# Optimization experiments

Hardware: AMD Instinct MI355X
Metric: run time of the kernel (lower is better)

The kernel has to match this reference:

```python
import jax, jax.numpy as jnp
import numpy as np

B, T, C, H, W = 16, 8, 2048, 16, 8
C8, C4, HW, NP = C // 8, C // 4, H * W, T // 2


def _cbr(x, w, s, b):
    # 1x1 conv + folded BN (eval-mode affine) + ReLU; x: (N, Cin, H, W), w: (Cout, Cin)
    y = jnp.einsum('oc,nchw->nohw', w, x)
    return jax.nn.relu(y * s[None, :, None, None] + b[None, :, None, None])


def setup_inputs():
    key = jax.random.key(0)
    ks = jax.random.split(key, 16)
    r = lambda i, shape, sc: jax.random.normal(ks[i], shape, jnp.float32) * sc
    return dict(
        featmap=r(0, (B, T, C, H, W), 1.0),
        re_featmap=r(1, (B * T, C, H, W), 1.0),
        vect_featmap=r(2, (B, T, C), 1.0),
        embed_feat=r(3, (B, T, 128, H, W), 1.0),
        gamma_w=r(4, (C8, C), 0.03), gamma_s=jnp.ones((C8,)), gamma_b=jnp.zeros((C8,)),
        beta_w=r(5, (C8, C), 0.03), beta_s=jnp.ones((C8,)), beta_b=jnp.zeros((C8,)),
        gg_w=r(6, (128, 2 * HW), 0.05), gg_s=jnp.ones((128,)), gg_b=jnp.zeros((128,)),
        tte_w=r(7, (128, 256), 0.05), tte_s=jnp.ones((128,)), tte_b=jnp.zeros((128,)),
        te_w=r(8, (1, 256), 0.05), te_s=jnp.ones((1,)), te_b=jnp.zeros((1,)),
        theta_w=r(9, (C8, C), 0.03), theta_b=jnp.zeros((C8,)),
        cp_w1=r(10, (C8, C4), 0.05), cp_b1=jnp.zeros((C8,)),
        cp_w2=r(11, (C, C8), 0.05), cp_b2=jnp.zeros((C,)),
    )


def reference(featmap, re_featmap, vect_featmap, embed_feat,
              gamma_w, gamma_s, gamma_b, beta_w, beta_s, beta_b,
              gg_w, gg_s, gg_b, tte_w, tte_s, tte_b, te_w, te_s, te_b,
              theta_w, theta_b, cp_w1, cp_b1, cp_w2, cp_b2):
    # spatial attention embeddings: (B, T, C8, HW)
    gamma = _cbr(re_featmap, gamma_w, gamma_s, gamma_b).reshape(B, T, C8, HW)
    beta = _cbr(re_featmap, beta_w, beta_s, beta_b).reshape(B, T, C8, HW)

    # channel attention: Conv1d over time of (B, C, T) -> (B, C8, T)
    cp = jax.nn.relu(jnp.einsum('oc,btc->bot', theta_w, vect_featmap) + theta_b[None, :, None])
    cp = cp.reshape(B, C8, NP, 2)
    c0 = cp[..., 0].transpose(0, 2, 1)  # (B, NP, C8)
    c1 = cp[..., 1].transpose(0, 2, 1)

    def mlp(x):  # (B, NP, C4) -> sigmoid gate (B, NP, C)
        h1 = jax.nn.relu(x @ cp_w1.T + cp_b1)
        return jax.nn.sigmoid(h1 @ cp_w2.T + cp_b2)

    p00 = mlp(jnp.concatenate([c0, c1], -1))  # (B, NP, C)
    p01 = mlp(jnp.concatenate([c1, c0], -1))

    # pairwise spatial graphs
    g0, g1 = gamma[:, 0::2], gamma[:, 1::2]  # (B, NP, C8, HW)
    b0, b1 = beta[:, 0::2], beta[:, 1::2]
    Gs0 = jnp.einsum('bpcs,bpct->bpst', g0, b1)  # (B, NP, HW, HW)
    Gs1 = jnp.einsum('bpcs,bpct->bpst', g1, b0)
    # Gs_in = Gs^T viewed as (HW, H, W); Gs_out = Gs viewed likewise
    j0 = jnp.concatenate([Gs0.transpose(0, 1, 3, 2), Gs1], 2).reshape(B * NP, 2 * HW, H, W)
    j1 = jnp.concatenate([Gs1.transpose(0, 1, 3, 2), Gs0], 2).reshape(B * NP, 2 * HW, H, W)
    gj0 = _cbr(j0, gg_w, gg_s, gg_b)  # (B*NP, 128, H, W)
    gj1 = _cbr(j1, gg_w, gg_s, gg_b)

    ef = embed_feat.reshape(B, NP, 2, 128, H, W)
    e0 = ef[:, :, 0].reshape(B * NP, 128, H, W)
    e1 = ef[:, :, 1].reshape(B * NP, 128, H, W)
    ta = _cbr(jnp.concatenate([e0, e1], 1), tte_w, tte_s, tte_b)  # (B*NP, 128, H, W)
    tb = _cbr(jnp.concatenate([e1, e0], 1), tte_w, tte_s, tte_b)

    def gate(t_feat, gj):  # conv 256->1 + BN + sigmoid
        y = jnp.einsum('oc,nchw->nohw', te_w, jnp.concatenate([t_feat, gj], 1))
        return jax.nn.sigmoid(y * te_s[None, :, None, None] + te_b[None, :, None, None])

    pa = gate(ta, gj0).reshape(B, NP, 1, H, W)
    pb = gate(tb, gj1).reshape(B, NP, 1, H, W)

    f = featmap.reshape(B, NP, 2, C, H, W)
    gate0 = p00[..., None, None] * pa  # (B, NP, C, H, W)
    gate1 = p01[..., None, None] * pb
    out = jax.nn.relu(gate0 * f[:, :, 0] + gate1 * f[:, :, 1])
    return out * out  # (B, T//2, C, H, W)
```

## Files before the change

### kernel.cpp

```cpp
#include <hip/hip_runtime.h>
#include <stdint.h>


typedef _Float16 f16;
typedef _Float16 f16x8 __attribute__((ext_vector_type(8)));
typedef float f32x4 __attribute__((ext_vector_type(4)));

typedef const void __attribute__((address_space(1)))* gptr1;
typedef void __attribute__((address_space(3)))* lptr3;

__device__ __forceinline__ void gload16(const void* g, void* l) {
  __builtin_amdgcn_global_load_lds((gptr1)g, (lptr3)l, 16, 0, 0);
}

__device__ __forceinline__ float sigmoidf_(float x) { return 1.f / (1.f + expf(-x)); }

#define WAIT_VM6 asm volatile("s_waitcnt vmcnt(6)" ::: "memory")
#define WAIT_VM0 asm volatile("s_waitcnt vmcnt(0)" ::: "memory")
#define WAIT_LGKM8 asm volatile("s_waitcnt lgkmcnt(8)" ::: "memory")
#define WAIT_LGKM0 asm volatile("s_waitcnt lgkmcnt(0)" ::: "memory")

__global__ __launch_bounds__(256) void kPP(const float* __restrict__ x,
                                           f16* __restrict__ Af,
                                           const float* __restrict__ gw, const float* __restrict__ gs,
                                           const float* __restrict__ bw, const float* __restrict__ bs,
                                           const float* __restrict__ gg_w, const float* __restrict__ gg_s,
                                           const float* __restrict__ tte_w, const float* __restrict__ tte_s,
                                           const float* __restrict__ thw, const float* __restrict__ w1,
                                           const float* __restrict__ w2,
                                           f16* __restrict__ Wf,
                                           float* __restrict__ ggT, float* __restrict__ tteT,
                                           float* __restrict__ thwT, float* __restrict__ w1T,
                                           float* __restrict__ w2T) {
  __shared__ __align__(16) char shmem[64 * 129 * 4];
  int t = threadIdx.x;
  int bid = blockIdx.x;
  if (bid < 4096) {
    float (*L)[129] = (float(*)[129])shmem;
    int n = bid >> 5;
    int k0 = (bid & 31) * 64;
    const float* src = x + (size_t)n * 262144 + (size_t)k0 * 128;
    for (int r = 0; r < 8; ++r) {
      int f = r * 256 + t;
      int kk = f >> 5, c4 = (f & 31) * 4;
      float4 v = *(const float4*)(src + kk * 128 + c4);
      L[kk][c4 + 0] = v.x; L[kk][c4 + 1] = v.y; L[kk][c4 + 2] = v.z; L[kk][c4 + 3] = v.w;
    }
    __syncthreads();
    for (int r = 0; r < 4; ++r) {
      int id = r * 256 + t;
      int hw = id >> 3, c = id & 7;
      int cs = c ^ (hw & 7);
      f16x8 h8;
      for (int j = 0; j < 8; ++j)
        h8[j] = (f16)L[cs * 8 + j][hw];
      size_t m = (size_t)n * 128 + hw;
      size_t ob = m * 2048 + (size_t)k0 + (size_t)c * 8;
      *(f16x8*)(Af + ob) = h8;
    }
    return;
  }
  if (bid < 4608) {
    int id = (bid - 4096) * 256 + t;
    int o = id >> 8, cch = id & 255;
    float s; const float* row;
    if (o < 256) { s = gs[o]; row = gw + (size_t)o * 2048; }
    else         { s = bs[o - 256]; row = bw + (size_t)(o - 256) * 2048; }
    int kb = cch >> 3, sub = cch & 7;
    int subd = sub ^ (o & 7);
    f16x8 h8;
    for (int j = 0; j < 8; ++j)
      h8[j] = (f16)(row[cch * 8 + j] * s);
    size_t ob = (size_t)o * 2048 + (size_t)kb * 64 + (size_t)subd * 8;
    *(f16x8*)(Wf + ob) = h8;
    return;
  }
  float (*TL)[65] = (float(*)[65])shmem;
  int tb = bid - 4608;
  const float* src; float* dst; const float* scale = nullptr; int R, C;
  if (tb < 128)      { src = thw;   dst = thwT; R = 256;  C = 2048; }
  else if (tb < 256) { tb -= 128; src = w2;  dst = w2T;  R = 2048; C = 256; }
  else if (tb < 288) { tb -= 256; src = w1;  dst = w1T;  R = 256;  C = 512; }
  else if (tb < 296) { tb -= 288; src = gg_w;  dst = ggT;  scale = gg_s;  R = 128; C = 256; }
  else               { tb -= 296; src = tte_w; dst = tteT; scale = tte_s; R = 128; C = 256; }
  int tpc = C >> 6;
  int r0 = (tb / tpc) * 64, c0 = (tb % tpc) * 64;
  int i16 = t >> 4, j4 = (t & 15) * 4;
  for (int s = 0; s < 4; ++s) {
    int i = i16 + s * 16;
    float4 v = *(const float4*)(src + (size_t)(r0 + i) * C + c0 + j4);
    TL[i][j4 + 0] = v.x; TL[i][j4 + 1] = v.y; TL[i][j4 + 2] = v.z; TL[i][j4 + 3] = v.w;
  }
  __syncthreads();
  for (int s = 0; s < 4; ++s) {
    int j = i16 + s * 16;
    float4 w;
    w.x = TL[j4 + 0][j]; w.y = TL[j4 + 1][j]; w.z = TL[j4 + 2][j]; w.w = TL[j4 + 3][j];
    if (scale) {
      w.x *= scale[r0 + j4 + 0]; w.y *= scale[r0 + j4 + 1];
      w.z *= scale[r0 + j4 + 2]; w.w *= scale[r0 + j4 + 3];
    }
    *(float4*)(dst + (size_t)(c0 + j) * R + r0 + j4) = w;
  }
}

__global__ __launch_bounds__(512, 2) void kGemm8(const f16* __restrict__ Af, const f16* __restrict__ Wf,
                                                 const float* __restrict__ gamma_b, const float* __restrict__ beta_b,
                                                 float* __restrict__ gammaF, float* __restrict__ betaF) {
  __shared__ __align__(16) f16 S[3][24576];
  int t = threadIdx.x;
  int lane = t & 63, wid = t >> 6;
  int wr = wid >> 2, wc = wid & 3;
  int bid = blockIdx.x;
  int bx = (bid & 7) * 16 + (bid >> 4);
  int by = (bid >> 3) & 1;
  size_t M0 = (size_t)bx * 128;
  size_t N0 = (size_t)by * 256;
  int row8 = wid * 8 + (lane >> 3);
  int sl = lane & 7;
  int fr = lane & 15, fq = lane >> 4;
  f32x4 acc[4][4] = {};
  f16x8 a[8], b[8];

  const char* AB = (const char*)Af;
  const char* WB = (const char*)Wf;
  const size_t aoff0 = (M0 + row8) * 4096 + (size_t)sl * 16;
  const size_t aoff1 = (M0 + 64 + row8) * 4096 + (size_t)sl * 16;
  const size_t woff0 = (N0 + row8) * 4096 + (size_t)sl * 16;
  const size_t woff1 = (N0 + 64 + row8) * 4096 + (size_t)sl * 16;
  const size_t woff2 = (N0 + 128 + row8) * 4096 + (size_t)sl * 16;
  const size_t woff3 = (N0 + 192 + row8) * 4096 + (size_t)sl * 16;

#define STAGE_ALL(dst, s) do {                                                     \
    int koff_ = (s) << 7;                                                          \
    char* l_ = (char*)(dst) + wid * 1024;                                          \
    gload16(AB + aoff0 + koff_, l_);                                               \
    gload16(AB + aoff1 + koff_, l_ + 8192);                                        \
    gload16(WB + woff0 + koff_, l_ + 16384);                                       \
    gload16(WB + woff1 + koff_, l_ + 24576);                                       \
    gload16(WB + woff2 + koff_, l_ + 32768);                                       \
    gload16(WB + woff3 + koff_, l_ + 40960);                                       \
  } while (0)

#define LOADG(buf, g) do {                                                         \
    const f16* bA_ = (const f16*)(buf);                                            \
    const f16* bB_ = bA_ + 8192;                                                   \
    int cg_ = (g) * 4 + fq;                                                        \
    _Pragma("unroll") for (int mi = 0; mi < 4; ++mi) {                             \
      int m_ = wr * 64 + mi * 16 + fr;                                             \
      a[(g) * 4 + mi] = *(const f16x8*)(bA_ + m_ * 64 + ((cg_ ^ (m_ & 7)) << 3));  \
    }                                                                              \
    _Pragma("unroll") for (int ni = 0; ni < 4; ++ni) {                             \
      int n_ = wc * 64 + ni * 16 + fr;                                             \
      b[(g) * 4 + ni] = *(const f16x8*)(bB_ + n_ * 64 + ((cg_ ^ (n_ & 7)) << 3));  \
    }                                                                              \
  } while (0)

#define STEP(rdbuf, stbuf, kt) do {                                                \
    if ((kt) < 31) { WAIT_VM6; } else { WAIT_VM0; }                                \
    __builtin_amdgcn_s_barrier();                                                  \
    if ((kt) <= 29) STAGE_ALL(stbuf, (kt) + 2);                                    \
    LOADG(rdbuf, 0);                                                               \
    __builtin_amdgcn_sched_barrier(0);                                             \
    LOADG(rdbuf, 1);                                                               \
    WAIT_LGKM8;                                                                    \
    __builtin_amdgcn_sched_barrier(0);                                             \
    __builtin_amdgcn_s_setprio(1);                                                 \
    _Pragma("unroll") for (int mi = 0; mi < 4; ++mi)                               \
      _Pragma("unroll") for (int ni = 0; ni < 4; ++ni)                             \
        acc[mi][ni] = __builtin_amdgcn_mfma_f32_16x16x32_f16(a[mi], b[ni], acc[mi][ni], 0, 0, 0); \
    WAIT_LGKM0;                                                                    \
    __builtin_amdgcn_sched_barrier(0);                                             \
    _Pragma("unroll") for (int mi = 0; mi < 4; ++mi)                               \
      _Pragma("unroll") for (int ni = 0; ni < 4; ++ni)                             \
        acc[mi][ni] = __builtin_amdgcn_mfma_f32_16x16x32_f16(a[4 + mi], b[4 + ni], acc[mi][ni], 0, 0, 0); \
    __builtin_amdgcn_s_setprio(0);                                                 \
  } while (0)

  STAGE_ALL(&S[0][0], 0);
  STAGE_ALL(&S[1][0], 1);
  for (int base = 0; base < 30; base += 3) {
    STEP(&S[0][0], &S[2][0], base);
    STEP(&S[1][0], &S[0][0], base + 1);
    STEP(&S[2][0], &S[1][0], base + 2);
  }
  STEP(&S[0][0], &S[2][0], 30);
  STEP(&S[1][0], &S[0][0], 31);
#undef STEP
#undef LOADG
#undef STAGE_ALL

  const float* bias = by ? beta_b : gamma_b;
  float* outb = by ? betaF : gammaF;
#pragma unroll
  for (int mi = 0; mi < 4; ++mi) {
    int hwb = wr * 64 + mi * 16 + fq * 4;
#pragma unroll
    for (int ni = 0; ni < 4; ++ni) {
      int o = wc * 64 + ni * 16 + fr;
      float bb = bias[o];
      f32x4 v = acc[mi][ni];
      float4 w;
      w.x = fmaxf(v[0] + bb, 0.f);
      w.y = fmaxf(v[1] + bb, 0.f);
      w.z = fmaxf(v[2] + bb, 0.f);
      w.w = fmaxf(v[3] + bb, 0.f);
      *(float4*)(outb + (size_t)bx * 32768 + (size_t)o * 128 + hwb) = w;
    }
  }
}

__global__ __launch_bounds__(256) void kTT(const float* __restrict__ vect, const float* __restrict__ thwT,
                                           float* __restrict__ P,
                                           const float* __restrict__ embed, const float* __restrict__ tteT,
                                           const float* __restrict__ tte_b, const float* __restrict__ te_w,
                                           float* __restrict__ Sta) {
  __shared__ float V[512];
  __shared__ __align__(16) float E[256 * 64];
  __shared__ float Red[16 * 64];
  int bid = blockIdx.x;
  int t = threadIdx.x;
  if (bid < 512) {
    int bt = bid & 127, kq = bid >> 7;
    const float* src = vect + (size_t)bt * 2048 + kq * 512;
    if (t < 128) *(float4*)(V + t * 4) = *(const float4*)(src + t * 4);
    __syncthreads();
    const float* wp = thwT + (size_t)kq * 512 * 256 + t;
    float acc = 0.f;
#pragma unroll 8
    for (int c = 0; c < 512; ++c)
      acc = fmaf(wp[(size_t)c * 256], V[c], acc);
    P[((size_t)kq * 128 + bt) * 256 + t] = acc;
    return;
  }
  int i = bid - 512;
  int n = i & 63, gate = (i >> 6) & 1, hh = (i >> 7) & 1;
  int b = n >> 2, p = n & 3;
  const float* eA = embed + (size_t)(b * 8 + 2 * p + gate) * 16384 + hh * 64;
  const float* eB = embed + (size_t)(b * 8 + 2 * p + 1 - gate) * 16384 + hh * 64;
  for (int r = 0; r < 8; ++r) {
    int f = r * 256 + t;
    int ch = f >> 4, q = (f & 15) * 4;
    *(float4*)(E + ch * 64 + q) = *(const float4*)(eA + (size_t)ch * 128 + q);
  }
  for (int r = 0; r < 8; ++r) {
    int f = r * 256 + t;
    int ch = f >> 4, q = (f & 15) * 4;
    *(float4*)(E + (128 + ch) * 64 + q) = *(const float4*)(eB + (size_t)ch * 128 + q);
  }
  __syncthreads();
  int ty = t >> 4, tx = t & 15;
  float acc[8][4] = {};
  for (int c = 0; c < 256; ++c) {
    float w8[8];
    *(float4*)w8 = *(const float4*)(tteT + (size_t)c * 128 + ty * 8);
    *(float4*)(w8 + 4) = *(const float4*)(tteT + (size_t)c * 128 + ty * 8 + 4);
    float4 g = *(const float4*)(E + c * 64 + tx * 4);
    for (int ii = 0; ii < 8; ++ii) {
      acc[ii][0] = fmaf(w8[ii], g.x, acc[ii][0]);
      acc[ii][1] = fmaf(w8[ii], g.y, acc[ii][1]);
      acc[ii][2] = fmaf(w8[ii], g.z, acc[ii][2]);
      acc[ii][3] = fmaf(w8[ii], g.w, acc[ii][3]);
    }
  }
  float par[4] = {0.f, 0.f, 0.f, 0.f};
  for (int ii = 0; ii < 8; ++ii) {
    int o = ty * 8 + ii;
    float tb = tte_b[o], tw = te_w[o];
    for (int j = 0; j < 4; ++j)
      par[j] += tw * fmaxf(acc[ii][j] + tb, 0.f);
  }
  for (int j = 0; j < 4; ++j) Red[ty * 64 + tx * 4 + j] = par[j];
  __syncthreads();
  if (t < 64) {
    float s = 0.f;
    for (int g = 0; g < 16; ++g) s += Red[g * 64 + t];
    Sta[(size_t)gate * 8192 + n * 128 + hh * 64 + t] = s;
  }
}

__global__ __launch_bounds__(256) void kAG(const float* __restrict__ P, const float* __restrict__ thb,
                                           const float* __restrict__ w1T, const float* __restrict__ b1,
                                           float* __restrict__ h1,
                                           const float* __restrict__ gammaF, const float* __restrict__ betaF,
                                           float* __restrict__ Gs0, float* __restrict__ Gs1) {
  __shared__ float x0[256], x1[256];
  __shared__ float ra[256], rb[256];
  __shared__ __align__(16) float As[16 * 128];
  __shared__ __align__(16) float Bs[16 * 64];
  int bid = blockIdx.x;
  int t = threadIdx.x;
  if (bid < 256) {
    int bp = bid & 63, och = bid >> 6;
    int b = bp >> 2, p = bp & 3;
    int bt0 = b * 8 + 2 * p, bt1 = bt0 + 1;
    {
      float a0 = 0.f, a1 = 0.f;
      for (int q = 0; q < 4; ++q) {
        a0 += P[((size_t)q * 128 + bt0) * 256 + t];
        a1 += P[((size_t)q * 128 + bt1) * 256 + t];
      }
      float tb = thb[t];
      x0[t] = fmaxf(a0 + tb, 0.f);
      x1[t] = fmaxf(a1 + tb, 0.f);
    }
    __syncthreads();
    int o = och * 64 + (t & 63);
    int ks = t >> 6;
    const float* xa = (ks < 2) ? x0 : x1;
    const float* xb = (ks < 2) ? x1 : x0;
    int kbase = ks * 128;
    int xoff = (ks < 2) ? kbase : kbase - 256;
    float aa = 0.f, ab = 0.f;
#pragma unroll 8
    for (int ii = 0; ii < 128; ++ii) {
      float w = w1T[(size_t)(kbase + ii) * 256 + o];
      aa = fmaf(w, xa[xoff + ii], aa);
      ab = fmaf(w, xb[xoff + ii], ab);
    }
    ra[t] = aa;
    rb[t] = ab;
    __syncthreads();
    if (t < 64) {
      float sa = ra[t] + ra[64 + t] + ra[128 + t] + ra[192 + t];
      float sb = rb[t] + rb[64 + t] + rb[128 + t] + rb[192 + t];
      float bb = b1[o];
      h1[((size_t)bp * 2) * 256 + o] = fmaxf(sa + bb, 0.f);
      h1[((size_t)bp * 2 + 1) * 256 + o] = fmaxf(sb + bb, 0.f);
    }
    return;
  }
  int i = bid - 256;
  int n = i & 63, which = (i >> 6) & 1, th = (i >> 7) & 1;
  int b = n >> 2, p = n & 3;
  int tg = 2 * p + which;
  int tb = 2 * p + 1 - which;
  const float* A = gammaF + (size_t)(b * 8 + tg) * 32768;
  const float* Bm = betaF + (size_t)(b * 8 + tb) * 32768;
  float* out = (which ? Gs1 : Gs0) + (size_t)n * 16384;
  int ty = t >> 4, tx = t & 15;
  float acc[8][4] = {};
  for (int c0 = 0; c0 < 256; c0 += 16) {
    for (int r = 0; r < 2; ++r) {
      int f = r * 256 + t;
      int cc = f >> 5, col = (f & 31) * 4;
      *(float4*)(As + cc * 128 + col) = *(const float4*)(A + (size_t)(c0 + cc) * 128 + col);
    }
    {
      int cc = t >> 4, col = (t & 15) * 4;
      *(float4*)(Bs + cc * 64 + col) = *(const float4*)(Bm + (size_t)(c0 + cc) * 128 + th * 64 + col);
    }
    __syncthreads();
    for (int cc = 0; cc < 16; ++cc) {
      float a8[8];
      *(float4*)a8 = *(const float4*)(As + cc * 128 + ty * 8);
      *(float4*)(a8 + 4) = *(const float4*)(As + cc * 128 + ty * 8 + 4);
      float4 b4 = *(const float4*)(Bs + cc * 64 + tx * 4);
      for (int ii = 0; ii < 8; ++ii) {
        acc[ii][0] = fmaf(a8[ii], b4.x, acc[ii][0]);
        acc[ii][1] = fmaf(a8[ii], b4.y, acc[ii][1]);
        acc[ii][2] = fmaf(a8[ii], b4.z, acc[ii][2]);
        acc[ii][3] = fmaf(a8[ii], b4.w, acc[ii][3]);
      }
    }
    __syncthreads();
  }
  for (int ii = 0; ii < 8; ++ii) {
    *(float4*)(out + (size_t)(ty * 8 + ii) * 128 + th * 64 + tx * 4) =
        make_float4(acc[ii][0], acc[ii][1], acc[ii][2], acc[ii][3]);
  }
}

__global__ __launch_bounds__(256) void kBG(const float* __restrict__ h1, const float* __restrict__ w2T,
                                           const float* __restrict__ b2,
                                           float* __restrict__ p00, float* __restrict__ p01,
                                           const float* __restrict__ Gs0, const float* __restrict__ Gs1,
                                           const float* __restrict__ ggT, const float* __restrict__ gg_b,
                                           const float* __restrict__ te_w, float* __restrict__ Sgj) {
  __shared__ float ha[256], hb[256];
  __shared__ float G0h[64 * 129];
  __shared__ __align__(16) float G1c[128 * 64];
  __shared__ float Red[16 * 64];
  int bid = blockIdx.x;
  int t = threadIdx.x;
  if (bid < 512) {
    int bp = bid & 63, chc = bid >> 6;
    ha[t] = h1[((size_t)bp * 2) * 256 + t];
    hb[t] = h1[((size_t)bp * 2 + 1) * 256 + t];
    __syncthreads();
    int ch = chc * 256 + t;
    float sa = 0.f, sb = 0.f;
#pragma unroll 8
    for (int k = 0; k < 256; ++k) {
      float w = w2T[(size_t)k * 2048 + ch];
      sa = fmaf(w, ha[k], sa);
      sb = fmaf(w, hb[k], sb);
    }
    p00[(size_t)bp * 2048 + ch] = sigmoidf_(sa + b2[ch]);
    p01[(size_t)bp * 2048 + ch] = sigmoidf_(sb + b2[ch]);
    return;
  }
  int i = bid - 512;
  int n = i & 63, gate = (i >> 6) & 1, hh = (i >> 7) & 1;
  const float* srcT = (gate == 0 ? Gs0 : Gs1) + (size_t)n * 16384;
  const float* srcC = (gate == 0 ? Gs1 : Gs0) + (size_t)n * 16384;
  for (int r = 0; r < 8; ++r) {
    int f = r * 256 + t;
    int hwl = f >> 5, c4 = (f & 31) * 4;
    float4 v = *(const float4*)(srcT + (size_t)(hh * 64 + hwl) * 128 + c4);
    G0h[hwl * 129 + c4 + 0] = v.x;
    G0h[hwl * 129 + c4 + 1] = v.y;
    G0h[hwl * 129 + c4 + 2] = v.z;
    G0h[hwl * 129 + c4 + 3] = v.w;
  }
  for (int r = 0; r < 8; ++r) {
    int f = r * 256 + t;
    int c = f >> 4, q = (f & 15) * 4;
    *(float4*)(G1c + c * 64 + q) = *(const float4*)(srcC + (size_t)c * 128 + hh * 64 + q);
  }
  __syncthreads();
  int ty = t >> 4, tx = t & 15;
  float acc[8][4] = {};
  for (int c = 0; c < 128; ++c) {
    float w8[8];
    *(float4*)w8 = *(const float4*)(ggT + (size_t)c * 128 + ty * 8);
    *(float4*)(w8 + 4) = *(const float4*)(ggT + (size_t)c * 128 + ty * 8 + 4);
    float g4[4];
    for (int j = 0; j < 4; ++j) g4[j] = G0h[(tx * 4 + j) * 129 + c];
    for (int ii = 0; ii < 8; ++ii)
      for (int j = 0; j < 4; ++j)
        acc[ii][j] = fmaf(w8[ii], g4[j], acc[ii][j]);
  }
  for (int c = 0; c < 128; ++c) {
    float w8[8];
    *(float4*)w8 = *(const float4*)(ggT + (size_t)(128 + c) * 128 + ty * 8);
    *(float4*)(w8 + 4) = *(const float4*)(ggT + (size_t)(128 + c) * 128 + ty * 8 + 4);
    float4 g = *(const float4*)(G1c + c * 64 + tx * 4);
    for (int ii = 0; ii < 8; ++ii) {
      acc[ii][0] = fmaf(w8[ii], g.x, acc[ii][0]);
      acc[ii][1] = fmaf(w8[ii], g.y, acc[ii][1]);
      acc[ii][2] = fmaf(w8[ii], g.z, acc[ii][2]);
      acc[ii][3] = fmaf(w8[ii], g.w, acc[ii][3]);
    }
  }
  float par[4] = {0.f, 0.f, 0.f, 0.f};
  for (int ii = 0; ii < 8; ++ii) {
    int o = ty * 8 + ii;
    float gb = gg_b[o], tw = te_w[128 + o];
    for (int j = 0; j < 4; ++j)
      par[j] += tw * fmaxf(acc[ii][j] + gb, 0.f);
  }
  for (int j = 0; j < 4; ++j) Red[ty * 64 + tx * 4 + j] = par[j];
  __syncthreads();
  if (t < 64) {
    float s = 0.f;
    for (int g = 0; g < 16; ++g) s += Red[g * 64 + t];
    Sgj[(size_t)gate * 8192 + n * 128 + hh * 64 + t] = s;
  }
}

__global__ __launch_bounds__(256) void kFinal(const float* __restrict__ featmap, const float* __restrict__ p00,
                                              const float* __restrict__ p01, const float* __restrict__ Sta,
                                              const float* __restrict__ Sgj, const float* __restrict__ te_s,
                                              const float* __restrict__ te_b, float* __restrict__ out) {
  int fid = blockIdx.x * 256 + threadIdx.x;
  int h4 = (fid & 31) * 4;
  int c = (fid >> 5) & 2047;
  int bp = fid >> 16;
  int b = bp >> 2, p = bp & 3;
  float ga = p00[(size_t)bp * 2048 + c];
  float gb = p01[(size_t)bp * 2048 + c];
  float ts = te_s[0], tbv = te_b[0];
  float4 sa0 = *(const float4*)(Sta + (size_t)bp * 128 + h4);
  float4 sg0 = *(const float4*)(Sgj + (size_t)bp * 128 + h4);
  float4 sa1 = *(const float4*)(Sta + 8192 + (size_t)bp * 128 + h4);
  float4 sg1 = *(const float4*)(Sgj + 8192 + (size_t)bp * 128 + h4);
  float4 pa4, pb4;
  pa4.x = sigmoidf_(ts * (sa0.x + sg0.x) + tbv);
  pa4.y = sigmoidf_(ts * (sa0.y + sg0.y) + tbv);
  pa4.z = sigmoidf_(ts * (sa0.z + sg0.z) + tbv);
  pa4.w = sigmoidf_(ts * (sa0.w + sg0.w) + tbv);
  pb4.x = sigmoidf_(ts * (sa1.x + sg1.x) + tbv);
  pb4.y = sigmoidf_(ts * (sa1.y + sg1.y) + tbv);
  pb4.z = sigmoidf_(ts * (sa1.z + sg1.z) + tbv);
  pb4.w = sigmoidf_(ts * (sa1.w + sg1.w) + tbv);
  const float* f0 = featmap + (size_t)(b * 8 + 2 * p) * 262144 + (size_t)c * 128 + h4;
  const float* f1 = f0 + 262144;
  float4 v0 = *(const float4*)f0;
  float4 v1 = *(const float4*)f1;
  float4 o4;
  float r;
  r = fmaxf(ga * pa4.x * v0.x + gb * pb4.x * v1.x, 0.f); o4.x = r * r;
  r = fmaxf(ga * pa4.y * v0.y + gb * pb4.y * v1.y, 0.f); o4.y = r * r;
  r = fmaxf(ga * pa4.z * v0.z + gb * pb4.z * v1.z, 0.f); o4.z = r * r;
  r = fmaxf(ga * pa4.w * v0.w + gb * pb4.w * v1.w, 0.f); o4.w = r * r;
  *(float4*)(out + (size_t)fid * 4) = o4;
}

extern "C" void kernel_launch(void* const* d_in, const int* in_sizes, int n_in,
                              void* d_out, int out_size, void* d_ws, size_t ws_size,
                              hipStream_t stream) {
  (void)in_sizes; (void)n_in; (void)out_size; (void)ws_size;
  const float* featmap    = (const float*)d_in[0];
  const float* re_featmap = (const float*)d_in[1];
  const float* vect       = (const float*)d_in[2];
  const float* embed      = (const float*)d_in[3];
  const float* gamma_w    = (const float*)d_in[4];
  const float* gamma_s    = (const float*)d_in[5];
  const float* gamma_b    = (const float*)d_in[6];
  const float* beta_w     = (const float*)d_in[7];
  const float* beta_s     = (const float*)d_in[8];
  const float* beta_b     = (const float*)d_in[9];
  const float* gg_w       = (const float*)d_in[10];
  const float* gg_s       = (const float*)d_in[11];
  const float* gg_b       = (const float*)d_in[12];
  const float* tte_w      = (const float*)d_in[13];
  const float* tte_s      = (const float*)d_in[14];
  const float* tte_b      = (const float*)d_in[15];
  const float* te_w       = (const float*)d_in[16];
  const float* te_s       = (const float*)d_in[17];
  const float* te_b       = (const float*)d_in[18];
  const float* theta_w    = (const float*)d_in[19];
  const float* theta_b    = (const float*)d_in[20];
  const float* cp_w1      = (const float*)d_in[21];
  const float* cp_b1      = (const float*)d_in[22];
  const float* cp_w2      = (const float*)d_in[23];
  const float* cp_b2      = (const float*)d_in[24];
  float* out = (float*)d_out;

  char* w = (char*)d_ws;
  f16* Af  = (f16*)w;   w += (size_t)16384 * 2048 * 2;
  f16* Wf  = (f16*)w;   w += (size_t)512 * 2048 * 2;
  float* gammaF = (float*)w; w += (size_t)128 * 256 * 128 * 4;
  float* betaF  = (float*)w; w += (size_t)128 * 256 * 128 * 4;
  float* Gs0    = (float*)w; w += (size_t)64 * 128 * 128 * 4;
  float* Gs1    = (float*)w; w += (size_t)64 * 128 * 128 * 4;
  float* ggT    = (float*)w; w += (size_t)256 * 128 * 4;
  float* tteT   = (float*)w; w += (size_t)256 * 128 * 4;
  float* thwT   = (float*)w; w += (size_t)2048 * 256 * 4;
  float* w1T    = (float*)w; w += (size_t)512 * 256 * 4;
  float* w2T    = (float*)w; w += (size_t)256 * 2048 * 4;
  float* P      = (float*)w; w += (size_t)4 * 128 * 256 * 4;
  float* h1     = (float*)w; w += (size_t)64 * 2 * 256 * 4;
  float* Sta    = (float*)w; w += (size_t)2 * 64 * 128 * 4;
  float* Sgj    = (float*)w; w += (size_t)2 * 64 * 128 * 4;
  float* p00    = (float*)w; w += (size_t)64 * 2048 * 4;
  float* p01    = (float*)w; w += (size_t)64 * 2048 * 4;

  kPP<<<4912, 256, 0, stream>>>(re_featmap, Af,
                                gamma_w, gamma_s, beta_w, beta_s, gg_w, gg_s, tte_w, tte_s,
                                theta_w, cp_w1, cp_w2, Wf, ggT, tteT, thwT, w1T, w2T);
  kGemm8<<<256, 512, 0, stream>>>(Af, Wf, gamma_b, beta_b, gammaF, betaF);
  kTT<<<768, 256, 0, stream>>>(vect, thwT, P, embed, tteT, tte_b, te_w, Sta);
  kAG<<<512, 256, 0, stream>>>(P, theta_b, w1T, cp_b1, h1, gammaF, betaF, Gs0, Gs1);
  kBG<<<768, 256, 0, stream>>>(h1, w2T, cp_b2, p00, p01, Gs0, Gs1, ggT, gg_b, te_w, Sgj);
  kFinal<<<16384, 256, 0, stream>>>(featmap, p00, p01, Sta, Sgj, te_s, te_b, out);
}
```

Measured before the change: 246.0 us.

## Double-buffer MFMA fragment registers to overlap LDS reads with compute in GEMM

Restructures the kGemm8 main loop so fragments for the next K-tile are read from LDS into a second register bank while MFMAs run on the current bank. This replaces the earlier split-half lgkmcnt waits and the prio/sched barriers. Global offsets are also narrowed to 32-bit to cut address arithmetic. The cost is double the fragment registers, which puts pressure on the 2-wave-per-SIMD occupancy target. It also waits on vmcnt(0) every step, which shortens the effective prefetch depth of the global loads.

```diff
diff --git a/kernel.cpp b/kernel.cpp
--- a/kernel.cpp
+++ b/kernel.cpp
@@ -17,8 +17,6 @@
 
 #define WAIT_VM6 asm volatile("s_waitcnt vmcnt(6)" ::: "memory")
 #define WAIT_VM0 asm volatile("s_waitcnt vmcnt(0)" ::: "memory")
-#define WAIT_LGKM8 asm volatile("s_waitcnt lgkmcnt(8)" ::: "memory")
-#define WAIT_LGKM0 asm volatile("s_waitcnt lgkmcnt(0)" ::: "memory")
 
 __global__ __launch_bounds__(256) void kPP(const float* __restrict__ x,
                                            f16* __restrict__ Af,
@@ -120,19 +118,19 @@
   int sl = lane & 7;
   int fr = lane & 15, fq = lane >> 4;
   f32x4 acc[4][4] = {};
-  f16x8 a[8], b[8];
+  f16x8 a0[8], b0[8], a1[8], b1[8];
 
   const char* AB = (const char*)Af;
   const char* WB = (const char*)Wf;
-  const size_t aoff0 = (M0 + row8) * 4096 + (size_t)sl * 16;
-  const size_t aoff1 = (M0 + 64 + row8) * 4096 + (size_t)sl * 16;
-  const size_t woff0 = (N0 + row8) * 4096 + (size_t)sl * 16;
-  const size_t woff1 = (N0 + 64 + row8) * 4096 + (size_t)sl * 16;
-  const size_t woff2 = (N0 + 128 + row8) * 4096 + (size_t)sl * 16;
-  const size_t woff3 = (N0 + 192 + row8) * 4096 + (size_t)sl * 16;
+  const uint32_t aoff0 = (uint32_t)((M0 + row8) * 4096) + sl * 16;
+  const uint32_t aoff1 = (uint32_t)((M0 + 64 + row8) * 4096) + sl * 16;
+  const uint32_t woff0 = (uint32_t)((N0 + row8) * 4096) + sl * 16;
+  const uint32_t woff1 = (uint32_t)((N0 + 64 + row8) * 4096) + sl * 16;
+  const uint32_t woff2 = (uint32_t)((N0 + 128 + row8) * 4096) + sl * 16;
+  const uint32_t woff3 = (uint32_t)((N0 + 192 + row8) * 4096) + sl * 16;
 
 #define STAGE_ALL(dst, s) do {                                                     \
-    int koff_ = (s) << 7;                                                          \
+    uint32_t koff_ = (uint32_t)(s) << 7;                                           \
     char* l_ = (char*)(dst) + wid * 1024;                                          \
     gload16(AB + aoff0 + koff_, l_);                                               \
     gload16(AB + aoff1 + koff_, l_ + 8192);                                        \
@@ -142,51 +140,60 @@
     gload16(WB + woff3 + koff_, l_ + 40960);                                       \
   } while (0)
 
-#define LOADG(buf, g) do {                                                         \
+#define LOADG(buf, A_, B_) do {                                                    \
     const f16* bA_ = (const f16*)(buf);                                            \
     const f16* bB_ = bA_ + 8192;                                                   \
-    int cg_ = (g) * 4 + fq;                                                        \
-    _Pragma("unroll") for (int mi = 0; mi < 4; ++mi) {                             \
-      int m_ = wr * 64 + mi * 16 + fr;                                             \
-      a[(g) * 4 + mi] = *(const f16x8*)(bA_ + m_ * 64 + ((cg_ ^ (m_ & 7)) << 3));  \
-    }                                                                              \
-    _Pragma("unroll") for (int ni = 0; ni < 4; ++ni) {                             \
-      int n_ = wc * 64 + ni * 16 + fr;                                             \
-      b[(g) * 4 + ni] = *(const f16x8*)(bB_ + n_ * 64 + ((cg_ ^ (n_ & 7)) << 3));  \
+    _Pragma("unroll") for (int g = 0; g < 2; ++g) {                                \
+      int cg_ = g * 4 + fq;                                                        \
+      _Pragma("unroll") for (int mi = 0; mi < 4; ++mi) {                           \
+        int m_ = wr * 64 + mi * 16 + fr;                                           \
+        A_[g * 4 + mi] = *(const f16x8*)(bA_ + m_ * 64 + ((cg_ ^ (m_ & 7)) << 3)); \
+      }                                                                            \
+      _Pragma("unroll") for (int ni = 0; ni < 4; ++ni) {                           \
+        int n_ = wc * 64 + ni * 16 + fr;                                           \
+        B_[g * 4 + ni] = *(const f16x8*)(bB_ + n_ * 64 + ((cg_ ^ (n_ & 7)) << 3)); \
+      }                                                                            \
     }                                                                              \
   } while (0)
 
-#define STEP(rdbuf, stbuf, kt) do {                                                \
-    if ((kt) < 31) { WAIT_VM6; } else { WAIT_VM0; }                                \
+#define MFMA_BANK(A_, B_) do {                                                     \
+    _Pragma("unroll") for (int g = 0; g < 2; ++g)                                  \
+      _Pragma("unroll") for (int mi = 0; mi < 4; ++mi)                             \
+        _Pragma("unroll") for (int ni = 0; ni < 4; ++ni)                           \
+          acc[mi][ni] = __builtin_amdgcn_mfma_f32_16x16x32_f16(                    \
+              A_[g * 4 + mi], B_[g * 4 + ni], acc[mi][ni], 0, 0, 0);               \
+  } while (0)
+
+#define STEP(rdbuf, stbuf, sdata, CA, CB, NA, NB) do {                             \
+    WAIT_VM0;                                                                      \
     __builtin_amdgcn_s_barrier();                                                  \
-    if ((kt) <= 29) STAGE_ALL(stbuf, (kt) + 2);                                    \
-    LOADG(rdbuf, 0);                                                               \
-    __builtin_amdgcn_sched_barrier(0);                                             \
-    LOADG(rdbuf, 1);                                                               \
-    WAIT_LGKM8;                                                                    \
-    __builtin_amdgcn_sched_barrier(0);                                             \
-    __builtin_amdgcn_s_setprio(1);                                                 \
-    _Pragma("unroll") for (int mi = 0; mi < 4; ++mi)                               \
-      _Pragma("unroll") for (int ni = 0; ni < 4; ++ni)                             \
-        acc[mi][ni] = __builtin_amdgcn_mfma_f32_16x16x32_f16(a[mi], b[ni], acc[mi][ni], 0, 0, 0); \
-    WAIT_LGKM0;                                                                    \
-    __builtin_amdgcn_sched_barrier(0);                                             \
-    _Pragma("unroll") for (int mi = 0; mi < 4; ++mi)                               \
-      _Pragma("unroll") for (int ni = 0; ni < 4; ++ni)                             \
-        acc[mi][ni] = __builtin_amdgcn_mfma_f32_16x16x32_f16(a[4 + mi], b[4 + ni], acc[mi][ni], 0, 0, 0); \
-    __builtin_amdgcn_s_setprio(0);                                                 \
+    STAGE_ALL(stbuf, sdata);                                                       \
+    LOADG(rdbuf, NA, NB);                                                          \
+    MFMA_BANK(CA, CB);                                                             \
   } while (0)
 
   STAGE_ALL(&S[0][0], 0);
   STAGE_ALL(&S[1][0], 1);
-  for (int base = 0; base < 30; base += 3) {
-    STEP(&S[0][0], &S[2][0], base);
-    STEP(&S[1][0], &S[0][0], base + 1);
-    STEP(&S[2][0], &S[1][0], base + 2);
-  }
-  STEP(&S[0][0], &S[2][0], 30);
-  STEP(&S[1][0], &S[0][0], 31);
+  WAIT_VM6;
+  __builtin_amdgcn_s_barrier();
+  LOADG(&S[0][0], a0, b0);
+
+  for (int it = 0; it < 5; ++it) {
+    int k6 = it * 6;
+    STEP(&S[1][0], &S[2][0], k6 + 2, a0, b0, a1, b1);
+    STEP(&S[2][0], &S[0][0], k6 + 3, a1, b1, a0, b0);
+    STEP(&S[0][0], &S[1][0], k6 + 4, a0, b0, a1, b1);
+    STEP(&S[1][0], &S[2][0], k6 + 5, a1, b1, a0, b0);
+    STEP(&S[2][0], &S[0][0], k6 + 6, a0, b0, a1, b1);
+    STEP(&S[0][0], &S[1][0], k6 + 7, a1, b1, a0, b0);
+  }
+  WAIT_VM0;
+  __builtin_amdgcn_s_barrier();
+  LOADG(&S[1][0], a1, b1);
+  MFMA_BANK(a0, b0);
+  MFMA_BANK(a1, b1);
 #undef STEP
+#undef MFMA_BANK
 #undef LOADG
 #undef STAGE_ALL
 
```

New measurement: 252.3 us. +2.5%, slower.
